# Performance work log

Hardware: AMD Instinct MI355X
Metric: run time of the kernel (lower is better)

The kernel has to match this reference:

```python
import jax, jax.numpy as jnp
import numpy as np

N = 100000   # num nodes
E = 600000   # num edges (avg degree 6)
H = 8        # num_heads
D = 16       # out_dim
T = 20000    # minibatch target nodes


def setup_inputs() -> dict:
    key = jax.random.key(0)
    k1, k2, k3, k4 = jax.random.split(key, 4)
    node = jax.random.normal(k1, (N, H, D), dtype=jnp.float32)
    eft = jax.random.normal(k2, (E, H, D), dtype=jnp.float32)
    dst = jax.random.randint(k3, (E,), 0, N, dtype=jnp.int32)
    target_idx = jax.random.randint(k4, (T,), 0, N, dtype=jnp.int32)
    return {"node": node, "eft": eft, "dst": dst, "target_idx": target_idx}


def reference(node, eft, dst, target_idx):
    # e_mul_v: edge feature * gathered destination node feature, [E,H,D]
    m = eft * node[dst]
    sim = m.sum(axis=-1)                              # [E,H]
    # NOTE: forward applies F.softmax over dim=-1 (the HEADS axis), per source.
    a = jax.nn.softmax(sim, axis=-1)[..., None]        # [E,H,1]
    # message passing: scatter-sum of eft * a into destination nodes
    nft = jax.ops.segment_sum(eft * a, dst, num_segments=node.shape[0])  # [N,H,D]
    v = nft.reshape(-1, H, D)
    x = v[target_idx] + 1e-15                           # [T,H,D]
    # F.normalize(x, 2): L2-normalize over dim=1 (heads), eps=1e-12
    norm = jnp.sqrt(jnp.sum(x * x, axis=1, keepdims=True))
    out = x / jnp.maximum(norm, 1e-12)
    return out, a
```

## Files before the change

### kernel.cpp

```cpp
#include <hip/hip_runtime.h>
#include <math.h>

#define HH 8
#define DD 16
#define HD 128
#define CAP 64

typedef float fx2 __attribute__((ext_vector_type(2)));
typedef int   ix4 __attribute__((ext_vector_type(4)));

__global__ void __launch_bounds__(256) mark_kernel(
    const int* __restrict__ tidx,
    unsigned char* __restrict__ mark,
    int T)
{
    int t = blockIdx.x * blockDim.x + threadIdx.x;
    if (t < T) mark[tidx[t]] = 1;
}

__global__ void __launch_bounds__(256) edge_kernel(
    const float* __restrict__ node,
    const float* __restrict__ eft,
    const int*   __restrict__ dst,
    const unsigned char* __restrict__ mark,
    int*         __restrict__ counts,
    int*         __restrict__ elist,
    float*       __restrict__ a_out,
    int E)
{
    const int lane   = threadIdx.x & 63;
    const int wid    = (int)((blockIdx.x * blockDim.x + threadIdx.x) >> 6);
    const int nwaves = (int)((gridDim.x * blockDim.x) >> 6);

    for (int base = wid * 4; base < E; base += nwaves * 4) {
        if (base + 3 < E) {
            ix4 d4 = __builtin_nontemporal_load((const ix4*)(dst + base));
            int dn0 = __builtin_amdgcn_readfirstlane(d4.x);
            int dn1 = __builtin_amdgcn_readfirstlane(d4.y);
            int dn2 = __builtin_amdgcn_readfirstlane(d4.z);
            int dn3 = __builtin_amdgcn_readfirstlane(d4.w);

            const fx2* ep = (const fx2*)(eft + (size_t)base * HD);
            fx2 ev0 = __builtin_nontemporal_load(ep + lane);
            fx2 ev1 = __builtin_nontemporal_load(ep + 64 + lane);
            fx2 ev2 = __builtin_nontemporal_load(ep + 128 + lane);
            fx2 ev3 = __builtin_nontemporal_load(ep + 192 + lane);
            float2 nv0 = ((const float2*)(node + (size_t)dn0 * HD))[lane];
            float2 nv1 = ((const float2*)(node + (size_t)dn1 * HD))[lane];
            float2 nv2 = ((const float2*)(node + (size_t)dn2 * HD))[lane];
            float2 nv3 = ((const float2*)(node + (size_t)dn3 * HD))[lane];

            float p0 = ev0.x * nv0.x + ev0.y * nv0.y;
            float p1 = ev1.x * nv1.x + ev1.y * nv1.y;
            float p2 = ev2.x * nv2.x + ev2.y * nv2.y;
            float p3 = ev3.x * nv3.x + ev3.y * nv3.y;
            p0 += __shfl_xor(p0, 1); p1 += __shfl_xor(p1, 1);
            p2 += __shfl_xor(p2, 1); p3 += __shfl_xor(p3, 1);
            p0 += __shfl_xor(p0, 2); p1 += __shfl_xor(p1, 2);
            p2 += __shfl_xor(p2, 2); p3 += __shfl_xor(p3, 2);
            p0 += __shfl_xor(p0, 4); p1 += __shfl_xor(p1, 4);
            p2 += __shfl_xor(p2, 4); p3 += __shfl_xor(p3, 4);

            float x0 = __expf(p0), x1 = __expf(p1);
            float x2 = __expf(p2), x3 = __expf(p3);
            float s0 = x0, s1 = x1, s2 = x2, s3 = x3;
            s0 += __shfl_xor(s0, 8);  s1 += __shfl_xor(s1, 8);
            s2 += __shfl_xor(s2, 8);  s3 += __shfl_xor(s3, 8);
            s0 += __shfl_xor(s0, 16); s1 += __shfl_xor(s1, 16);
            s2 += __shfl_xor(s2, 16); s3 += __shfl_xor(s3, 16);
            s0 += __shfl_xor(s0, 32); s1 += __shfl_xor(s1, 32);
            s2 += __shfl_xor(s2, 32); s3 += __shfl_xor(s3, 32);
            float a0 = __fdividef(x0, s0);
            float a1 = __fdividef(x1, s1);
            float a2 = __fdividef(x2, s2);
            float a3 = __fdividef(x3, s3);

            if ((lane & 7) == 0) {
                int h = lane >> 3;
                float* ap = a_out + (size_t)base * HH + h;
                ap[0]  = a0;
                ap[8]  = a1;
                ap[16] = a2;
                ap[24] = a3;
            }

            unsigned char mk0 = mark[dn0];
            unsigned char mk1 = mark[dn1];
            unsigned char mk2 = mark[dn2];
            unsigned char mk3 = mark[dn3];
            int mydn = (lane == 1) ? dn1 : (lane == 2) ? dn2 : (lane == 3) ? dn3 : dn0;
            unsigned char mymk = (lane == 1) ? mk1 : (lane == 2) ? mk2 : (lane == 3) ? mk3 : mk0;
            if (lane < 4 && mymk) {
                int s = atomicAdd(counts + mydn, 1);
                if (s < CAP) elist[(size_t)mydn * CAP + s] = base + lane;
            }
        } else {
            for (int e = base; e < E; e++) {
                int dn = __builtin_amdgcn_readfirstlane(dst[e]);
                float2 ev = ((const float2*)(eft + (size_t)e * HD))[lane];
                float2 nv = ((const float2*)(node + (size_t)dn * HD))[lane];
                float p = ev.x * nv.x + ev.y * nv.y;
                p += __shfl_xor(p, 1);
                p += __shfl_xor(p, 2);
                p += __shfl_xor(p, 4);
                float ex = __expf(p);
                float s = ex;
                s += __shfl_xor(s, 8);
                s += __shfl_xor(s, 16);
                s += __shfl_xor(s, 32);
                float a = __fdividef(ex, s);
                if ((lane & 7) == 0)
                    a_out[(size_t)e * HH + (lane >> 3)] = a;
                if (mark[dn] && lane == 0) {
                    int sl = atomicAdd(counts + dn, 1);
                    if (sl < CAP) elist[(size_t)dn * CAP + sl] = e;
                }
            }
        }
    }
}

__global__ void __launch_bounds__(256) gather_kernel(
    const float* __restrict__ eft,
    const float* __restrict__ a_out,
    const int*   __restrict__ counts,
    const int*   __restrict__ elist,
    const int*   __restrict__ tidx,
    float*       __restrict__ out,
    int T)
{
    int w    = (int)((blockIdx.x * blockDim.x + threadIdx.x) >> 6);
    int lane = threadIdx.x & 63;
    if (w >= T) return;
    int n   = tidx[w];
    int cnt = counts[n];
    if (cnt > CAP) cnt = CAP;
    const int* el = elist + (size_t)n * CAP;

    float2 acc = make_float2(0.0f, 0.0f);
    int i = 0;
    for (; i + 1 < cnt; i += 2) {
        int e0 = el[i];
        int e1 = el[i + 1];
        float2 ev0 = ((const float2*)(eft + (size_t)e0 * HD))[lane];
        float2 ev1 = ((const float2*)(eft + (size_t)e1 * HD))[lane];
        float av0 = a_out[(size_t)e0 * HH + (lane >> 3)];
        float av1 = a_out[(size_t)e1 * HH + (lane >> 3)];
        acc.x += ev0.x * av0 + ev1.x * av1;
        acc.y += ev0.y * av0 + ev1.y * av1;
    }
    if (i < cnt) {
        int e0 = el[i];
        float2 ev0 = ((const float2*)(eft + (size_t)e0 * HD))[lane];
        float av0 = a_out[(size_t)e0 * HH + (lane >> 3)];
        acc.x += ev0.x * av0;
        acc.y += ev0.y * av0;
    }

    acc.x += 1e-15f;
    acc.y += 1e-15f;
    float sx = acc.x * acc.x;
    float sy = acc.y * acc.y;
    sx += __shfl_xor(sx, 8);  sy += __shfl_xor(sy, 8);
    sx += __shfl_xor(sx, 16); sy += __shfl_xor(sy, 16);
    sx += __shfl_xor(sx, 32); sy += __shfl_xor(sy, 32);
    float2 o;
    o.x = acc.x / fmaxf(sqrtf(sx), 1e-12f);
    o.y = acc.y / fmaxf(sqrtf(sy), 1e-12f);
    ((float2*)(out + (size_t)w * HD))[lane] = o;
}

extern "C" void kernel_launch(void* const* d_in, const int* in_sizes, int n_in,
                              void* d_out, int out_size, void* d_ws, size_t ws_size,
                              hipStream_t stream)
{
    const float* node = (const float*)d_in[0];
    const float* eft  = (const float*)d_in[1];
    const int*   dst  = (const int*)d_in[2];
    const int*   tidx = (const int*)d_in[3];

    const int N = in_sizes[0] / HD;
    const int E = in_sizes[2];
    const int T = in_sizes[3];

    float* out   = (float*)d_out;
    float* a_out = out + (size_t)T * HD;

    int* counts = (int*)d_ws;
    int* elist  = counts + N;

    unsigned char* mark = (unsigned char*)d_out;

    (void)hipMemsetAsync(mark, 0, (size_t)N, stream);
    (void)hipMemsetAsync(counts, 0, (size_t)N * sizeof(int), stream);

    {
        int blocks = (T + 255) / 256;
        mark_kernel<<<blocks, 256, 0, stream>>>(tidx, mark, T);
    }

    {
        int blocks = 2048;
        edge_kernel<<<blocks, 256, 0, stream>>>(node, eft, dst, mark, counts,
                                                elist, a_out, E);
    }

    {
        int blocks = (T + 3) / 4;
        gather_kernel<<<blocks, 256, 0, stream>>>(eft, a_out, counts, elist,
                                                  tidx, out, T);
    }
}
```

Baseline: 495.6 us.

## Process eight edges per wave, use DPP reductions, and merge workspace memsets

The edge kernel now handles eight edges per wave iteration instead of four, issuing more independent eft and node loads per wave to raise memory-level parallelism. Intra-row reductions switch from shuffles to DPP row operations where possible, and lanes 0-7 pick their destination via selects so one mark load per lane replaces serial per-edge mark loads. The mark array moves from the output buffer into the workspace, so the two memsets collapse into a single memset. This raises register pressure, which may reduce occupancy, and relies on N being a multiple of 4 for counts alignment.

Result: no change. 486.6 us (-1.8%).

```diff
diff --git a/kernel.cpp b/kernel.cpp
--- a/kernel.cpp
+++ b/kernel.cpp
@@ -8,6 +8,12 @@
 
 typedef float fx2 __attribute__((ext_vector_type(2)));
 typedef int   ix4 __attribute__((ext_vector_type(4)));
+
+template <int CTRL>
+__device__ __forceinline__ float dpp_sum(float v) {
+    int r = __builtin_amdgcn_update_dpp(0, __float_as_int(v), CTRL, 0xF, 0xF, true);
+    return v + __int_as_float(r);
+}
 
 __global__ void __launch_bounds__(256) mark_kernel(
     const int* __restrict__ tidx,
@@ -32,65 +38,99 @@
     const int wid    = (int)((blockIdx.x * blockDim.x + threadIdx.x) >> 6);
     const int nwaves = (int)((gridDim.x * blockDim.x) >> 6);
 
-    for (int base = wid * 4; base < E; base += nwaves * 4) {
-        if (base + 3 < E) {
-            ix4 d4 = __builtin_nontemporal_load((const ix4*)(dst + base));
-            int dn0 = __builtin_amdgcn_readfirstlane(d4.x);
-            int dn1 = __builtin_amdgcn_readfirstlane(d4.y);
-            int dn2 = __builtin_amdgcn_readfirstlane(d4.z);
-            int dn3 = __builtin_amdgcn_readfirstlane(d4.w);
+    for (int base = wid * 8; base < E; base += nwaves * 8) {
+        if (base + 7 < E) {
+            ix4 dA = __builtin_nontemporal_load((const ix4*)(dst + base));
+            ix4 dB = __builtin_nontemporal_load((const ix4*)(dst + base + 4));
 
             const fx2* ep = (const fx2*)(eft + (size_t)base * HD);
             fx2 ev0 = __builtin_nontemporal_load(ep + lane);
             fx2 ev1 = __builtin_nontemporal_load(ep + 64 + lane);
             fx2 ev2 = __builtin_nontemporal_load(ep + 128 + lane);
             fx2 ev3 = __builtin_nontemporal_load(ep + 192 + lane);
+            fx2 ev4 = __builtin_nontemporal_load(ep + 256 + lane);
+            fx2 ev5 = __builtin_nontemporal_load(ep + 320 + lane);
+            fx2 ev6 = __builtin_nontemporal_load(ep + 384 + lane);
+            fx2 ev7 = __builtin_nontemporal_load(ep + 448 + lane);
+
+            int dn0 = __builtin_amdgcn_readfirstlane(dA.x);
+            int dn1 = __builtin_amdgcn_readfirstlane(dA.y);
+            int dn2 = __builtin_amdgcn_readfirstlane(dA.z);
+            int dn3 = __builtin_amdgcn_readfirstlane(dA.w);
+            int dn4 = __builtin_amdgcn_readfirstlane(dB.x);
+            int dn5 = __builtin_amdgcn_readfirstlane(dB.y);
+            int dn6 = __builtin_amdgcn_readfirstlane(dB.z);
+            int dn7 = __builtin_amdgcn_readfirstlane(dB.w);
             float2 nv0 = ((const float2*)(node + (size_t)dn0 * HD))[lane];
             float2 nv1 = ((const float2*)(node + (size_t)dn1 * HD))[lane];
             float2 nv2 = ((const float2*)(node + (size_t)dn2 * HD))[lane];
             float2 nv3 = ((const float2*)(node + (size_t)dn3 * HD))[lane];
-
-            float p0 = ev0.x * nv0.x + ev0.y * nv0.y;
-            float p1 = ev1.x * nv1.x + ev1.y * nv1.y;
-            float p2 = ev2.x * nv2.x + ev2.y * nv2.y;
-            float p3 = ev3.x * nv3.x + ev3.y * nv3.y;
-            p0 += __shfl_xor(p0, 1); p1 += __shfl_xor(p1, 1);
-            p2 += __shfl_xor(p2, 1); p3 += __shfl_xor(p3, 1);
-            p0 += __shfl_xor(p0, 2); p1 += __shfl_xor(p1, 2);
-            p2 += __shfl_xor(p2, 2); p3 += __shfl_xor(p3, 2);
-            p0 += __shfl_xor(p0, 4); p1 += __shfl_xor(p1, 4);
-            p2 += __shfl_xor(p2, 4); p3 += __shfl_xor(p3, 4);
+            float2 nv4 = ((const float2*)(node + (size_t)dn4 * HD))[lane];
+            float2 nv5 = ((const float2*)(node + (size_t)dn5 * HD))[lane];
+            float2 nv6 = ((const float2*)(node + (size_t)dn6 * HD))[lane];
+            float2 nv7 = ((const float2*)(node + (size_t)dn7 * HD))[lane];
+
+            float p0 = ev0.x*nv0.x + ev0.y*nv0.y;
+            float p1 = ev1.x*nv1.x + ev1.y*nv1.y;
+            float p2 = ev2.x*nv2.x + ev2.y*nv2.y;
+            float p3 = ev3.x*nv3.x + ev3.y*nv3.y;
+            float p4 = ev4.x*nv4.x + ev4.y*nv4.y;
+            float p5 = ev5.x*nv5.x + ev5.y*nv5.y;
+            float p6 = ev6.x*nv6.x + ev6.y*nv6.y;
+            float p7 = ev7.x*nv7.x + ev7.y*nv7.y;
+
+            p0 = dpp_sum<0xB1>(p0); p1 = dpp_sum<0xB1>(p1);
+            p2 = dpp_sum<0xB1>(p2); p3 = dpp_sum<0xB1>(p3);
+            p4 = dpp_sum<0xB1>(p4); p5 = dpp_sum<0xB1>(p5);
+            p6 = dpp_sum<0xB1>(p6); p7 = dpp_sum<0xB1>(p7);
+            p0 = dpp_sum<0x4E>(p0); p1 = dpp_sum<0x4E>(p1);
+            p2 = dpp_sum<0x4E>(p2); p3 = dpp_sum<0x4E>(p3);
+            p4 = dpp_sum<0x4E>(p4); p5 = dpp_sum<0x4E>(p5);
+            p6 = dpp_sum<0x4E>(p6); p7 = dpp_sum<0x4E>(p7);
+            p0 = dpp_sum<0x141>(p0); p1 = dpp_sum<0x141>(p1);
+            p2 = dpp_sum<0x141>(p2); p3 = dpp_sum<0x141>(p3);
+            p4 = dpp_sum<0x141>(p4); p5 = dpp_sum<0x141>(p5);
+            p6 = dpp_sum<0x141>(p6); p7 = dpp_sum<0x141>(p7);
 
             float x0 = __expf(p0), x1 = __expf(p1);
             float x2 = __expf(p2), x3 = __expf(p3);
-            float s0 = x0, s1 = x1, s2 = x2, s3 = x3;
-            s0 += __shfl_xor(s0, 8);  s1 += __shfl_xor(s1, 8);
-            s2 += __shfl_xor(s2, 8);  s3 += __shfl_xor(s3, 8);
+            float x4 = __expf(p4), x5 = __expf(p5);
+            float x6 = __expf(p6), x7 = __expf(p7);
+            float s0 = dpp_sum<0x140>(x0), s1 = dpp_sum<0x140>(x1);
+            float s2 = dpp_sum<0x140>(x2), s3 = dpp_sum<0x140>(x3);
+            float s4 = dpp_sum<0x140>(x4), s5 = dpp_sum<0x140>(x5);
+            float s6 = dpp_sum<0x140>(x6), s7 = dpp_sum<0x140>(x7);
             s0 += __shfl_xor(s0, 16); s1 += __shfl_xor(s1, 16);
             s2 += __shfl_xor(s2, 16); s3 += __shfl_xor(s3, 16);
+            s4 += __shfl_xor(s4, 16); s5 += __shfl_xor(s5, 16);
+            s6 += __shfl_xor(s6, 16); s7 += __shfl_xor(s7, 16);
             s0 += __shfl_xor(s0, 32); s1 += __shfl_xor(s1, 32);
             s2 += __shfl_xor(s2, 32); s3 += __shfl_xor(s3, 32);
+            s4 += __shfl_xor(s4, 32); s5 += __shfl_xor(s5, 32);
+            s6 += __shfl_xor(s6, 32); s7 += __shfl_xor(s7, 32);
             float a0 = __fdividef(x0, s0);
             float a1 = __fdividef(x1, s1);
             float a2 = __fdividef(x2, s2);
             float a3 = __fdividef(x3, s3);
+            float a4 = __fdividef(x4, s4);
+            float a5 = __fdividef(x5, s5);
+            float a6 = __fdividef(x6, s6);
+            float a7 = __fdividef(x7, s7);
 
             if ((lane & 7) == 0) {
-                int h = lane >> 3;
-                float* ap = a_out + (size_t)base * HH + h;
-                ap[0]  = a0;
-                ap[8]  = a1;
-                ap[16] = a2;
-                ap[24] = a3;
+                float* ap = a_out + (size_t)base * HH + (lane >> 3);
+                ap[0]  = a0; ap[8]  = a1; ap[16] = a2; ap[24] = a3;
+                ap[32] = a4; ap[40] = a5; ap[48] = a6; ap[56] = a7;
             }
 
-            unsigned char mk0 = mark[dn0];
-            unsigned char mk1 = mark[dn1];
-            unsigned char mk2 = mark[dn2];
-            unsigned char mk3 = mark[dn3];
-            int mydn = (lane == 1) ? dn1 : (lane == 2) ? dn2 : (lane == 3) ? dn3 : dn0;
-            unsigned char mymk = (lane == 1) ? mk1 : (lane == 2) ? mk2 : (lane == 3) ? mk3 : mk0;
-            if (lane < 4 && mymk) {
+            int t0 = (lane & 1) ? dA.y : dA.x;
+            int t1 = (lane & 1) ? dA.w : dA.z;
+            int u0 = (lane & 1) ? dB.y : dB.x;
+            int u1 = (lane & 1) ? dB.w : dB.z;
+            int tA = (lane & 2) ? t1 : t0;
+            int tB = (lane & 2) ? u1 : u0;
+            int mydn = (lane & 4) ? tB : tA;
+            if (lane < 8 && mark[mydn]) {
                 int s = atomicAdd(counts + mydn, 1);
                 if (s < CAP) elist[(size_t)mydn * CAP + s] = base + lane;
             }
@@ -186,13 +226,11 @@
     float* out   = (float*)d_out;
     float* a_out = out + (size_t)T * HD;
 
-    int* counts = (int*)d_ws;
+    unsigned char* mark = (unsigned char*)d_ws;
+    int* counts = (int*)((char*)d_ws + N);
     int* elist  = counts + N;
 
-    unsigned char* mark = (unsigned char*)d_out;
-
-    (void)hipMemsetAsync(mark, 0, (size_t)N, stream);
-    (void)hipMemsetAsync(counts, 0, (size_t)N * sizeof(int), stream);
+    (void)hipMemsetAsync(d_ws, 0, (size_t)N * 5, stream);
 
     {
         int blocks = (T + 255) / 256;
```
